# Optimization experiments

Hardware: AMD Instinct MI355X
Metric: run time of the kernel (lower is better)

## Reference

```python
import jax, jax.numpy as jnp
import numpy as np

D = 256      # hidden_dim
NH = 8       # num_heads
DH = D // NH # head_dim = 32
K = 5        # base_kernel -> NA3D kernel (5,5,5), causal on axis 0 (time)
EPS = 1e-6


def _axis_idx(L, k, causal):
    """Per-axis NATTEN neighbor indices [L, k] and validity mask [L, k]."""
    i = jnp.arange(L)
    o = jnp.arange(k)
    if causal:
        idx = i[:, None] - (k - 1) + o[None, :]   # last k positions incl. self
        mask = idx >= 0
        idx = jnp.clip(idx, 0, L - 1)
    else:
        start = jnp.clip(i - k // 2, 0, L - k)     # window shifts at borders
        idx = start[:, None] + o[None, :]
        mask = jnp.ones((L, k), dtype=bool)
    return idx, mask


def _rmsnorm(x, w):
    return x * jax.lax.rsqrt(jnp.mean(x * x, axis=-1, keepdims=True) + EPS) * w


def _na3d(x, wq, bq, wk, bk, wv, bv, wo, bo):
    # x: [B, T, H, W, D]; neighborhood attention, causal in T.
    B, T, H, W, Dm = x.shape
    q = (x @ wq + bq).reshape(B, T, H, W, NH, DH)
    k = (x @ wk + bk).reshape(B, T, H, W, NH, DH)
    v = (x @ wv + bv).reshape(B, T, H, W, NH, DH)

    tidx, tmask = _axis_idx(T, K, True)
    hidx, _ = _axis_idx(H, K, False)
    widx, _ = _axis_idx(W, K, False)

    # Gather neighbor windows: [B, T, H, W, K, K, K, NH, DH]
    ti = tidx[:, None, None, :, None, None]
    hi = hidx[None, :, None, None, :, None]
    wi = widx[None, None, :, None, None, :]
    kn = k[:, ti, hi, wi].reshape(B, T, H, W, K ** 3, NH, DH)
    vn = v[:, ti, hi, wi].reshape(B, T, H, W, K ** 3, NH, DH)

    # Validity mask (only causal time axis masks anything): [T, H, W, K^3]
    mask = jnp.broadcast_to(tmask[:, None, None, :, None, None],
                            (T, H, W, K, K, K)).reshape(T, H, W, K ** 3)

    logits = jnp.einsum('bthwnd,bthwmnd->bthwnm', q, kn) * (DH ** -0.5)
    logits = jnp.where(mask[None, :, :, :, None, :], logits, -jnp.inf)
    attn = jax.nn.softmax(logits, axis=-1)
    out = jnp.einsum('bthwnm,bthwmnd->bthwnd', attn, vn).reshape(B, T, H, W, Dm)
    return out @ wo + bo


def setup_inputs() -> dict:
    key = jax.random.key(0)
    ks = jax.random.split(key, 14)
    w = lambda k_, shape: jax.random.normal(k_, shape, jnp.float32) * 0.02
    return {
        'x': jax.random.normal(ks[0], (1, 8, 16, 16, D), jnp.float32),
        'norm1_w': jnp.ones((D,), jnp.float32),
        'norm2_w': jnp.ones((D,), jnp.float32),
        'wq': w(ks[1], (D, D)), 'bq': jnp.zeros((D,), jnp.float32),
        'wk': w(ks[2], (D, D)), 'bk': jnp.zeros((D,), jnp.float32),
        'wv': w(ks[3], (D, D)), 'bv': jnp.zeros((D,), jnp.float32),
        'wo': w(ks[4], (D, D)), 'bo': jnp.zeros((D,), jnp.float32),
        'w1': w(ks[5], (D, 4 * D)),
        'w2': w(ks[6], (D, 4 * D)),
        'w3': w(ks[7], (4 * D, D)),
    }


def reference(x, norm1_w, norm2_w, wq, bq, wk, bk, wv, bv, wo, bo, w1, w2, w3):
    # residual NA block
    h = x + _na3d(_rmsnorm(x, norm1_w), wq, bq, wk, bk, wv, bv, wo, bo)
    # residual SwiGLU FFN block
    y = _rmsnorm(h, norm2_w)
    h = h + (jax.nn.silu(y @ w1) * (y @ w2)) @ w3
    return h
```

## Files before the change

kernel.cpp:

```cpp
#include <hip/hip_runtime.h>
#include <hip/hip_bf16.h>

typedef __attribute__((ext_vector_type(8))) __bf16 bf16x8;
typedef __attribute__((ext_vector_type(4))) __bf16 bf16x4;
typedef __attribute__((ext_vector_type(4))) short shortx4;
typedef __attribute__((ext_vector_type(4))) float f32x4;

#define D    256
#define FF   1024
#define NTOK 2048

__device__ __forceinline__ float ldf(const void* p, int i, bool isf32){
  return isf32 ? ((const float*)p)[i] : (float)(((const __bf16*)p)[i]);
}

__device__ __forceinline__ f32x4 mfma16x16x16bf16(bf16x4 a, bf16x4 b, f32x4 c){
#if __has_builtin(__builtin_amdgcn_mfma_f32_16x16x16_bf16)
  return __builtin_amdgcn_mfma_f32_16x16x16_bf16(a, b, c, 0, 0, 0);
#elif __has_builtin(__builtin_amdgcn_mfma_f32_16x16x16bf16_1k)
  return __builtin_amdgcn_mfma_f32_16x16x16bf16_1k(__builtin_bit_cast(shortx4, a),
                                                   __builtin_bit_cast(shortx4, b), c, 0, 0, 0);
#else
  asm volatile("v_mfma_f32_16x16x16_bf16 %0, %1, %2, %0" : "+v"(c) : "v"(a), "v"(b));
  return c;
#endif
}

struct MiscArgs { const void* x; const void* vec[6]; };
struct TPArgs { const void* src[7]; };

__global__ __launch_bounds__(256) void prep_kernel(MiscArgs a, TPArgs ta,
                                                   float* __restrict__ X,
                                                   float* __restrict__ VEC,
                                                   __bf16* __restrict__ WT,
                                                   __bf16* __restrict__ XN,
                                                   const unsigned int* __restrict__ tagp){
  __shared__ float tl[32][33];
  __shared__ float red[4];
  bool isf32 = (*tagp == 0x3F800000u);
  int b = blockIdx.x, tid = threadIdx.x;

  if (b < 1024){
    const void* src; int Kd, Nd, dstOff, tk, tn;
    if (b < 256){
      int mat = b >> 6, t = b & 63;
      src = ta.src[mat]; Kd = 256; Nd = 256; dstOff = mat*65536;
      tk = t >> 3; tn = t & 7;
    } else if (b < 768){
      int mat = (b - 256) >> 8, t = (b - 256) & 255;
      src = ta.src[4 + mat]; Kd = 256; Nd = 1024; dstOff = 262144 + mat*262144;
      tk = t >> 5; tn = t & 31;
    } else {
      int t = b - 768;
      src = ta.src[6]; Kd = 1024; Nd = 256; dstOff = 786432;
      tk = t >> 3; tn = t & 7;
    }
    int tx = tid & 31, ty = tid >> 5;
    int k0 = tk*32, n0 = tn*32;
    #pragma unroll
    for (int i = 0; i < 4; i++){
      int kk = ty + i*8;
      tl[kk][tx] = ldf(src, (k0 + kk)*Nd + n0 + tx, isf32);
    }
    __syncthreads();
    #pragma unroll
    for (int i = 0; i < 4; i++){
      int nn = ty + i*8;
      WT[dstOff + (n0 + nn)*Kd + k0 + tx] = (__bf16)tl[tx][nn];
    }
  } else if (b < 3072){
    int tok = b - 1024;
    int idx = tok*D + tid;
    float xv = ldf(a.x, idx, isf32);
    X[idx] = xv;
    float s = xv*xv;
    #pragma unroll
    for (int d = 32; d > 0; d >>= 1) s += __shfl_xor(s, d, 64);
    if ((tid & 63) == 0) red[tid >> 6] = s;
    __syncthreads();
    float tot = red[0]+red[1]+red[2]+red[3];
    float w = ldf(a.vec[0], tid, isf32);
    XN[idx] = (__bf16)(xv * rsqrtf(tot*(1.0f/D) + 1e-6f) * w);
  } else {
    for (int i = tid; i < 1536; i += 256)
      VEC[i] = ldf(a.vec[i >> 8], i & 255, isf32);
  }
}

__global__ __launch_bounds__(256) void rmsnorm_kernel(const float* __restrict__ x,
                                                      const float* __restrict__ w,
                                                      __bf16* __restrict__ out){
  int tok = blockIdx.x, tid = threadIdx.x;
  int idx = tok*D + tid;
  float xv = x[idx];
  float s = xv*xv;
  #pragma unroll
  for (int d = 32; d > 0; d >>= 1) s += __shfl_xor(s, d, 64);
  __shared__ float red[4];
  if ((tid & 63) == 0) red[tid >> 6] = s;
  __syncthreads();
  float tot = red[0]+red[1]+red[2]+red[3];
  out[idx] = (__bf16)(xv * rsqrtf(tot*(1.0f/D) + 1e-6f) * w[tid]);
}


__device__ __forceinline__ void stage256(const __bf16* __restrict__ src, int strideElems,
                                         __bf16* __restrict__ lds){
  int tid = threadIdx.x;
  #pragma unroll
  for (int c = 0; c < 8; c++){
    int s = (c*256 + tid) << 4;
    int row = s >> 9, col = s & 511;
    *(float4*)((char*)lds + row*512 + (col ^ ((row & 7) << 4))) =
      *(const float4*)((const char*)src + row*strideElems*2 + col);
  }
}
__device__ __forceinline__ bf16x8 lrd256(const __bf16* __restrict__ lds, int row, int cb){
  return *(const bf16x8*)((const char*)lds + row*512 + (cb ^ ((row & 7) << 4)));
}

__device__ __forceinline__ void stage128(const __bf16* __restrict__ src, int strideElems,
                                         __bf16* __restrict__ lds){
  int tid = threadIdx.x;
  #pragma unroll
  for (int c = 0; c < 4; c++){
    int s = (c*256 + tid) << 4;
    int row = s >> 8, col = s & 255;
    *(float4*)((char*)lds + row*256 + (col ^ ((row & 7) << 4))) =
      *(const float4*)((const char*)src + row*strideElems*2 + col);
  }
}
__device__ __forceinline__ bf16x8 lrd128(const __bf16* __restrict__ lds, int row, int cb){
  return *(const bf16x8*)((const char*)lds + row*256 + (cb ^ ((row & 7) << 4)));
}

__device__ __forceinline__ void mfma256(const __bf16* __restrict__ As, const __bf16* __restrict__ Bs,
                                        f32x4 acc[2][2], int wrow, int wcol, int q, int ln){
  #pragma unroll
  for (int ks = 0; ks < 8; ks++){
    int cb = ks*64 + q*16;
    bf16x8 a0 = lrd256(As, wrow*32      + ln, cb);
    bf16x8 a1 = lrd256(As, wrow*32 + 16 + ln, cb);
    bf16x8 b0 = lrd256(Bs, wcol*32      + ln, cb);
    bf16x8 b1 = lrd256(Bs, wcol*32 + 16 + ln, cb);
    acc[0][0] = __builtin_amdgcn_mfma_f32_16x16x32_bf16(a0, b0, acc[0][0], 0, 0, 0);
    acc[0][1] = __builtin_amdgcn_mfma_f32_16x16x32_bf16(a0, b1, acc[0][1], 0, 0, 0);
    acc[1][0] = __builtin_amdgcn_mfma_f32_16x16x32_bf16(a1, b0, acc[1][0], 0, 0, 0);
    acc[1][1] = __builtin_amdgcn_mfma_f32_16x16x32_bf16(a1, b1, acc[1][1], 0, 0, 0);
  }
}

#define GEMM_PROLOGUE \
  int tid = threadIdx.x; \
  int wave = tid >> 6, lane = tid & 63; \
  int wrow = wave & 1, wcol = wave >> 1; \
  int q = lane >> 4, ln = lane & 15; \
  (void)tid; \
  f32x4 acc[2][2]; \
  acc[0][0] = (f32x4){0,0,0,0}; acc[0][1] = (f32x4){0,0,0,0}; \
  acc[1][0] = (f32x4){0,0,0,0}; acc[1][1] = (f32x4){0,0,0,0};

__global__ __launch_bounds__(256) void qkv_kernel(const __bf16* __restrict__ xn,
                                                  const __bf16* __restrict__ WT,
                                                  const float* __restrict__ VEC,
                                                  __bf16* __restrict__ Qb,
                                                  __bf16* __restrict__ Kb,
                                                  __bf16* __restrict__ VTb){
  __shared__ __align__(16) __bf16 As[64][256];
  __shared__ __align__(16) __bf16 Bs[64][256];
  int m0 = blockIdx.x*64;
  int sel = blockIdx.y >> 2, n0 = (blockIdx.y & 3)*64;
  const __bf16* B = WT + sel*65536;
  const float* bias = VEC + 512 + sel*256;
  GEMM_PROLOGUE
  stage256(xn + m0*D, D, &As[0][0]);
  stage256(B  + n0*D, D, &Bs[0][0]);
  __syncthreads();
  mfma256(&As[0][0], &Bs[0][0], acc, wrow, wcol, q, ln);
  if (sel < 2){
    __bf16* O = (sel == 0) ? Qb : Kb;
    #pragma unroll
    for (int c = 0; c < 2; c++){
      int col = n0 + wcol*32 + c*16 + ln;
      float bv = bias[col];
      #pragma unroll
      for (int r = 0; r < 2; r++){
        #pragma unroll
        for (int i = 0; i < 4; i++){
          int m = m0 + wrow*32 + r*16 + q*4 + i;
          O[m*D + col] = (__bf16)(acc[r][c][i] + bv);
        }
      }
    }
  } else {
    #pragma unroll
    for (int c = 0; c < 2; c++){
      int col = n0 + wcol*32 + c*16 + ln;
      float bv = bias[col];
      #pragma unroll
      for (int r = 0; r < 2; r++){
        int mb = m0 + wrow*32 + r*16 + q*4;
        bf16x4 pk;
        #pragma unroll
        for (int i = 0; i < 4; i++) pk[i] = (__bf16)(acc[r][c][i] + bv);
        *(bf16x4*)&VTb[col*NTOK + mb] = pk;
      }
    }
  }
}

__global__ __launch_bounds__(256) void attn_kernel(const __bf16* __restrict__ Qb,
                                                   const __bf16* __restrict__ Kb,
                                                   const __bf16* __restrict__ VT,
                                                   __bf16* __restrict__ attn){
  int row = blockIdx.x;
  int tq = row >> 4, hq = row & 15;
  int g  = (blockIdx.y << 2) + (threadIdx.x >> 6);
  int lane = threadIdx.x & 63;
  int ln = lane & 15, qt = lane >> 4;

  int qbase = (tq << 8) + (hq << 4);
  int h0 = min(max(hq - 2, 0), 11);
  int tlo = max(tq - 4, 0);

  bf16x8 qf = *(const bf16x8*)&Qb[(qbase + ln)*D + g*32 + qt*8];

  int wstart = min(max(ln - 2, 0), 11);
  float msk[4];
  #pragma unroll
  for (int r = 0; r < 4; r++){
    int wk = qt*4 + r;
    msk[r] = (wk >= wstart && wk <= wstart + 4) ? 0.0f : -INFINITY;
  }

  const float sc = 0.17677669529663687f;
  float m_run = -INFINITY, l_run = 0.0f;
  f32x4 o0 = (f32x4){0,0,0,0}, o1 = (f32x4){0,0,0,0};
  f32x4 zero = (f32x4){0,0,0,0};

  for (int tp = tlo; tp <= tq; tp++){
    #pragma unroll
    for (int hp = 0; hp < 5; hp++){
      int kb0 = (tp << 8) + ((h0 + hp) << 4);
      bf16x8 kf = *(const bf16x8*)&Kb[(kb0 + ln)*D + g*32 + qt*8];
      f32x4 s = __builtin_amdgcn_mfma_f32_16x16x32_bf16(kf, qf, zero, 0, 0, 0);
      float sv0 = s[0]*sc + msk[0];
      float sv1 = s[1]*sc + msk[1];
      float sv2 = s[2]*sc + msk[2];
      float sv3 = s[3]*sc + msk[3];
      float tm = fmaxf(fmaxf(sv0, sv1), fmaxf(sv2, sv3));
      tm = fmaxf(tm, __shfl_xor(tm, 16, 64));
      tm = fmaxf(tm, __shfl_xor(tm, 32, 64));
      float mnew = fmaxf(m_run, tm);
      float rs = __expf(m_run - mnew);
      float p0 = __expf(sv0 - mnew), p1 = __expf(sv1 - mnew);
      float p2 = __expf(sv2 - mnew), p3 = __expf(sv3 - mnew);
      bf16x4 pa;
      pa[0] = (__bf16)p0; pa[1] = (__bf16)p1; pa[2] = (__bf16)p2; pa[3] = (__bf16)p3;
      l_run = l_run*rs + (float)pa[0] + (float)pa[1] + (float)pa[2] + (float)pa[3];
      #pragma unroll
      for (int i = 0; i < 4; i++){ o0[i] *= rs; o1[i] *= rs; }
      m_run = mnew;
      bf16x4 v0 = *(const bf16x4*)&VT[(g*32      + ln)*NTOK + kb0 + qt*4];
      bf16x4 v1 = *(const bf16x4*)&VT[(g*32 + 16 + ln)*NTOK + kb0 + qt*4];
      o0 = mfma16x16x16bf16(v0, pa, o0);
      o1 = mfma16x16x16bf16(v1, pa, o1);
    }
  }
  l_run += __shfl_xor(l_run, 16, 64);
  l_run += __shfl_xor(l_run, 32, 64);
  float linv = 1.0f / l_run;
  int obase = (qbase + ln)*D + g*32;
  bf16x4 s0, s1;
  #pragma unroll
  for (int r = 0; r < 4; r++){
    s0[r] = (__bf16)(o0[r] * linv);
    s1[r] = (__bf16)(o1[r] * linv);
  }
  *(bf16x4*)&attn[obase      + qt*4] = s0;
  *(bf16x4*)&attn[obase + 16 + qt*4] = s1;
}

__global__ __launch_bounds__(256) void oproj_kernel(const __bf16* __restrict__ A,
                                                    const __bf16* __restrict__ WoT,
                                                    const float* __restrict__ VEC,
                                                    const float* __restrict__ X,
                                                    float* __restrict__ h){
  __shared__ __align__(16) __bf16 As[64][256];
  __shared__ __align__(16) __bf16 Bs[64][256];
  int m0 = blockIdx.x*64, n0 = blockIdx.y*64;
  GEMM_PROLOGUE
  stage256(A   + m0*D, D, &As[0][0]);
  stage256(WoT + n0*D, D, &Bs[0][0]);
  __syncthreads();
  mfma256(&As[0][0], &Bs[0][0], acc, wrow, wcol, q, ln);
  #pragma unroll
  for (int c = 0; c < 2; c++){
    int col = n0 + wcol*32 + c*16 + ln;
    float bv = VEC[1280 + col];
    #pragma unroll
    for (int r = 0; r < 2; r++){
      #pragma unroll
      for (int i = 0; i < 4; i++){
        int m = m0 + wrow*32 + r*16 + q*4 + i;
        int idx = m*D + col;
        h[idx] = acc[r][c][i] + bv + X[idx];
      }
    }
  }
}

__global__ __launch_bounds__(256) void ffn1_kernel(const __bf16* __restrict__ y,
                                                   const __bf16* __restrict__ W1T,
                                                   const __bf16* __restrict__ W2T,
                                                   __bf16* __restrict__ ffh){
  __shared__ __align__(16) __bf16 As [64][128];
  __shared__ __align__(16) __bf16 B1s[64][128];
  __shared__ __align__(16) __bf16 B2s[64][128];
  int m0 = blockIdx.x*64, n0 = blockIdx.y*64;
  int tid = threadIdx.x;
  int wave = tid >> 6, lane = tid & 63;
  int wrow = wave & 1, wcol = wave >> 1;
  int q = lane >> 4, ln = lane & 15;
  f32x4 acc1[2][2], acc2[2][2];
  #pragma unroll
  for (int r = 0; r < 2; r++)
    #pragma unroll
    for (int c = 0; c < 2; c++){ acc1[r][c] = (f32x4){0,0,0,0}; acc2[r][c] = (f32x4){0,0,0,0}; }

  #pragma unroll
  for (int k0 = 0; k0 < D; k0 += 128){
    if (k0) __syncthreads();
    stage128(y   + m0*D + k0, D, &As [0][0]);
    stage128(W1T + n0*D + k0, D, &B1s[0][0]);
    stage128(W2T + n0*D + k0, D, &B2s[0][0]);
    __syncthreads();
    #pragma unroll
    for (int ks = 0; ks < 4; ks++){
      int cb = ks*64 + q*16;
      bf16x8 a0 = lrd128(&As [0][0], wrow*32      + ln, cb);
      bf16x8 a1 = lrd128(&As [0][0], wrow*32 + 16 + ln, cb);
      bf16x8 p0 = lrd128(&B1s[0][0], wcol*32      + ln, cb);
      bf16x8 p1 = lrd128(&B1s[0][0], wcol*32 + 16 + ln, cb);
      bf16x8 u0 = lrd128(&B2s[0][0], wcol*32      + ln, cb);
      bf16x8 u1 = lrd128(&B2s[0][0], wcol*32 + 16 + ln, cb);
      acc1[0][0] = __builtin_amdgcn_mfma_f32_16x16x32_bf16(a0, p0, acc1[0][0], 0,0,0);
      acc1[0][1] = __builtin_amdgcn_mfma_f32_16x16x32_bf16(a0, p1, acc1[0][1], 0,0,0);
      acc1[1][0] = __builtin_amdgcn_mfma_f32_16x16x32_bf16(a1, p0, acc1[1][0], 0,0,0);
      acc1[1][1] = __builtin_amdgcn_mfma_f32_16x16x32_bf16(a1, p1, acc1[1][1], 0,0,0);
      acc2[0][0] = __builtin_amdgcn_mfma_f32_16x16x32_bf16(a0, u0, acc2[0][0], 0,0,0);
      acc2[0][1] = __builtin_amdgcn_mfma_f32_16x16x32_bf16(a0, u1, acc2[0][1], 0,0,0);
      acc2[1][0] = __builtin_amdgcn_mfma_f32_16x16x32_bf16(a1, u0, acc2[1][0], 0,0,0);
      acc2[1][1] = __builtin_amdgcn_mfma_f32_16x16x32_bf16(a1, u1, acc2[1][1], 0,0,0);
    }
  }
  #pragma unroll
  for (int c = 0; c < 2; c++){
    int col = n0 + wcol*32 + c*16 + ln;
    #pragma unroll
    for (int r = 0; r < 2; r++){
      #pragma unroll
      for (int i = 0; i < 4; i++){
        int m = m0 + wrow*32 + r*16 + q*4 + i;
        float gv = acc1[r][c][i], u = acc2[r][c][i];
        float sig = 1.0f / (1.0f + __expf(-gv));
        ffh[m*FF + col] = (__bf16)(gv * sig * u);
      }
    }
  }
}

__global__ __launch_bounds__(256) void ffn2_kernel(const __bf16* __restrict__ ffh,
                                                   const __bf16* __restrict__ W3T,
                                                   const float* __restrict__ h,
                                                   const unsigned int* __restrict__ tagp,
                                                   void* __restrict__ outp){
  __shared__ __align__(16) __bf16 As[64][256];
  __shared__ __align__(16) __bf16 Bs[64][256];
  int m0 = blockIdx.x*64, n0 = blockIdx.y*64;
  GEMM_PROLOGUE
  #pragma unroll
  for (int k0 = 0; k0 < FF; k0 += 256){
    if (k0) __syncthreads();
    stage256(ffh + m0*FF + k0, FF, &As[0][0]);
    stage256(W3T + n0*FF + k0, FF, &Bs[0][0]);
    __syncthreads();
    mfma256(&As[0][0], &Bs[0][0], acc, wrow, wcol, q, ln);
  }
  bool isf32 = (*tagp == 0x3F800000u);
  #pragma unroll
  for (int c = 0; c < 2; c++){
    int col = n0 + wcol*32 + c*16 + ln;
    #pragma unroll
    for (int r = 0; r < 2; r++){
      #pragma unroll
      for (int i = 0; i < 4; i++){
        int m = m0 + wrow*32 + r*16 + q*4 + i;
        int idx = m*D + col;
        float val = acc[r][c][i] + h[idx];
        if (isf32) ((float*)outp)[idx] = val;
        else       ((__bf16*)outp)[idx] = (__bf16)val;
      }
    }
  }
}

extern "C" void kernel_launch(void* const* d_in, const int* in_sizes, int n_in,
                              void* d_out, int out_size, void* d_ws, size_t ws_size,
                              hipStream_t stream){
  char* ws = (char*)d_ws;
  float*  X    = (float*)(ws);
  float*  VEC  = (float*)(ws + 2097152);
  __bf16* WT   = (__bf16*)(ws + 2097152 + 8192);
  __bf16* XN   = (__bf16*)(ws + 4202496);
  __bf16* Qb   = (__bf16*)(ws + 5251072);
  __bf16* Kb   = Qb + NTOK*D;
  __bf16* VTb  = Kb + NTOK*D;
  __bf16* ATT  = (__bf16*)(ws + 11542528);
  float*  Hb   = (float*)(ws + 12591104);
  __bf16* Yb   = (__bf16*)(ws + 14688256);
  __bf16* FFH  = (__bf16*)Qb;

  const unsigned int* tagp = (const unsigned int*)d_in[1];

  MiscArgs ma;
  ma.x = d_in[0];
  ma.vec[0] = d_in[1]; ma.vec[1] = d_in[2]; ma.vec[2] = d_in[4];
  ma.vec[3] = d_in[6]; ma.vec[4] = d_in[8]; ma.vec[5] = d_in[10];

  TPArgs ta;
  ta.src[0] = d_in[3];  ta.src[1] = d_in[5];  ta.src[2] = d_in[7];
  ta.src[3] = d_in[9];  ta.src[4] = d_in[11]; ta.src[5] = d_in[12];
  ta.src[6] = d_in[13];

  prep_kernel<<<3073, 256, 0, stream>>>(ma, ta, X, VEC, WT, XN, tagp);
  qkv_kernel<<<dim3(NTOK/64, 12), 256, 0, stream>>>(XN, WT, VEC, Qb, Kb, VTb);
  attn_kernel<<<dim3(128, 2), 256, 0, stream>>>(Qb, Kb, VTb, ATT);
  oproj_kernel<<<dim3(NTOK/64, 4), 256, 0, stream>>>(ATT, WT + 196608, VEC, X, Hb);
  rmsnorm_kernel<<<NTOK, 256, 0, stream>>>(Hb, VEC + 256, Yb);
  ffn1_kernel<<<dim3(NTOK/64, 16), 256, 0, stream>>>(Yb, WT + 262144, WT + 524288, FFH);
  ffn2_kernel<<<dim3(NTOK/64, 4), 256, 0, stream>>>(FFH, WT + 786432, Hb, tagp, d_out);
}
```

Measured before the change: 135.1 us.

## Fuse all stages into a cooperative persistent megakernel with grid syncs

Replaces the seven separate kernel launches with one cooperative kernel of 512 blocks that runs each stage in turn and separates them with grid-wide barriers. The goal is to remove per-launch overhead and the gaps between launches. In exchange every stage now runs under a fixed grid with 64KB of shared memory per block and launch bounds of 2 blocks per CU, so occupancy may drop. Grid syncs also cost time, and they can leave many blocks idle in stages with fewer tiles. If the cooperative launch fails, it falls back to the separate launches.

Measured after the change: 499.9 us. 270% more time.

```diff
diff --git a/kernel.cpp b/kernel.cpp
--- a/kernel.cpp
+++ b/kernel.cpp
@@ -1,5 +1,8 @@
 #include <hip/hip_runtime.h>
+#include <hip/hip_cooperative_groups.h>
 #include <hip/hip_bf16.h>
+
+namespace cg = cooperative_groups;
 
 typedef __attribute__((ext_vector_type(8))) __bf16 bf16x8;
 typedef __attribute__((ext_vector_type(4))) __bf16 bf16x4;
@@ -29,30 +32,32 @@
 struct MiscArgs { const void* x; const void* vec[6]; };
 struct TPArgs { const void* src[7]; };
 
-__global__ __launch_bounds__(256) void prep_kernel(MiscArgs a, TPArgs ta,
-                                                   float* __restrict__ X,
-                                                   float* __restrict__ VEC,
-                                                   __bf16* __restrict__ WT,
-                                                   __bf16* __restrict__ XN,
-                                                   const unsigned int* __restrict__ tagp){
-  __shared__ float tl[32][33];
-  __shared__ float red[4];
-  bool isf32 = (*tagp == 0x3F800000u);
-  int b = blockIdx.x, tid = threadIdx.x;
-
+struct MegaArgs {
+  MiscArgs ma; TPArgs ta;
+  float* X; float* VEC; __bf16* WT; __bf16* XN;
+  __bf16* Qb; __bf16* Kb; __bf16* VTb; __bf16* ATT;
+  float* Hb; __bf16* Yb; __bf16* FFH;
+  const unsigned int* tagp; void* out;
+};
+
+
+__device__ __forceinline__ void prep_body(const MegaArgs& A, int b, bool isf32, char* smem){
+  float (*tl)[33] = (float(*)[33])smem;
+  float* red = (float*)(smem + 4224);
+  int tid = threadIdx.x;
   if (b < 1024){
     const void* src; int Kd, Nd, dstOff, tk, tn;
     if (b < 256){
       int mat = b >> 6, t = b & 63;
-      src = ta.src[mat]; Kd = 256; Nd = 256; dstOff = mat*65536;
+      src = A.ta.src[mat]; Kd = 256; Nd = 256; dstOff = mat*65536;
       tk = t >> 3; tn = t & 7;
     } else if (b < 768){
       int mat = (b - 256) >> 8, t = (b - 256) & 255;
-      src = ta.src[4 + mat]; Kd = 256; Nd = 1024; dstOff = 262144 + mat*262144;
+      src = A.ta.src[4 + mat]; Kd = 256; Nd = 1024; dstOff = 262144 + mat*262144;
       tk = t >> 5; tn = t & 31;
     } else {
       int t = b - 768;
-      src = ta.src[6]; Kd = 1024; Nd = 256; dstOff = 786432;
+      src = A.ta.src[6]; Kd = 1024; Nd = 256; dstOff = 786432;
       tk = t >> 3; tn = t & 7;
     }
     int tx = tid & 31, ty = tid >> 5;
@@ -66,43 +71,40 @@
     #pragma unroll
     for (int i = 0; i < 4; i++){
       int nn = ty + i*8;
-      WT[dstOff + (n0 + nn)*Kd + k0 + tx] = (__bf16)tl[tx][nn];
+      A.WT[dstOff + (n0 + nn)*Kd + k0 + tx] = (__bf16)tl[tx][nn];
     }
   } else if (b < 3072){
     int tok = b - 1024;
     int idx = tok*D + tid;
-    float xv = ldf(a.x, idx, isf32);
-    X[idx] = xv;
+    float xv = ldf(A.ma.x, idx, isf32);
+    A.X[idx] = xv;
     float s = xv*xv;
     #pragma unroll
     for (int d = 32; d > 0; d >>= 1) s += __shfl_xor(s, d, 64);
     if ((tid & 63) == 0) red[tid >> 6] = s;
     __syncthreads();
     float tot = red[0]+red[1]+red[2]+red[3];
-    float w = ldf(a.vec[0], tid, isf32);
-    XN[idx] = (__bf16)(xv * rsqrtf(tot*(1.0f/D) + 1e-6f) * w);
+    float w = ldf(A.ma.vec[0], tid, isf32);
+    A.XN[idx] = (__bf16)(xv * rsqrtf(tot*(1.0f/D) + 1e-6f) * w);
   } else {
     for (int i = tid; i < 1536; i += 256)
-      VEC[i] = ldf(a.vec[i >> 8], i & 255, isf32);
-  }
-}
-
-__global__ __launch_bounds__(256) void rmsnorm_kernel(const float* __restrict__ x,
-                                                      const float* __restrict__ w,
-                                                      __bf16* __restrict__ out){
-  int tok = blockIdx.x, tid = threadIdx.x;
+      A.VEC[i] = ldf(A.ma.vec[i >> 8], i & 255, isf32);
+  }
+}
+
+__device__ __forceinline__ void rms2_body(const MegaArgs& A, int tok, char* smem){
+  float* red = (float*)smem;
+  int tid = threadIdx.x;
   int idx = tok*D + tid;
-  float xv = x[idx];
+  float xv = A.Hb[idx];
   float s = xv*xv;
   #pragma unroll
   for (int d = 32; d > 0; d >>= 1) s += __shfl_xor(s, d, 64);
-  __shared__ float red[4];
   if ((tid & 63) == 0) red[tid >> 6] = s;
   __syncthreads();
   float tot = red[0]+red[1]+red[2]+red[3];
-  out[idx] = (__bf16)(xv * rsqrtf(tot*(1.0f/D) + 1e-6f) * w[tid]);
-}
-
+  A.Yb[idx] = (__bf16)(xv * rsqrtf(tot*(1.0f/D) + 1e-6f) * A.VEC[256 + tid]);
+}
 
 __device__ __forceinline__ void stage256(const __bf16* __restrict__ src, int strideElems,
                                          __bf16* __restrict__ lds){
@@ -118,7 +120,6 @@
 __device__ __forceinline__ bf16x8 lrd256(const __bf16* __restrict__ lds, int row, int cb){
   return *(const bf16x8*)((const char*)lds + row*512 + (cb ^ ((row & 7) << 4)));
 }
-
 __device__ __forceinline__ void stage128(const __bf16* __restrict__ src, int strideElems,
                                          __bf16* __restrict__ lds){
   int tid = threadIdx.x;
@@ -133,7 +134,6 @@
 __device__ __forceinline__ bf16x8 lrd128(const __bf16* __restrict__ lds, int row, int cb){
   return *(const bf16x8*)((const char*)lds + row*256 + (cb ^ ((row & 7) << 4)));
 }
-
 __device__ __forceinline__ void mfma256(const __bf16* __restrict__ As, const __bf16* __restrict__ Bs,
                                         f32x4 acc[2][2], int wrow, int wcol, int q, int ln){
   #pragma unroll
@@ -160,25 +160,20 @@
   acc[0][0] = (f32x4){0,0,0,0}; acc[0][1] = (f32x4){0,0,0,0}; \
   acc[1][0] = (f32x4){0,0,0,0}; acc[1][1] = (f32x4){0,0,0,0};
 
-__global__ __launch_bounds__(256) void qkv_kernel(const __bf16* __restrict__ xn,
-                                                  const __bf16* __restrict__ WT,
-                                                  const float* __restrict__ VEC,
-                                                  __bf16* __restrict__ Qb,
-                                                  __bf16* __restrict__ Kb,
-                                                  __bf16* __restrict__ VTb){
-  __shared__ __align__(16) __bf16 As[64][256];
-  __shared__ __align__(16) __bf16 Bs[64][256];
-  int m0 = blockIdx.x*64;
-  int sel = blockIdx.y >> 2, n0 = (blockIdx.y & 3)*64;
-  const __bf16* B = WT + sel*65536;
-  const float* bias = VEC + 512 + sel*256;
+__device__ __forceinline__ void qkv_body(const MegaArgs& A, int bx, int by, char* smem){
+  __bf16* As = (__bf16*)smem;
+  __bf16* Bs = (__bf16*)(smem + 32768);
+  int m0 = bx*64;
+  int sel = by >> 2, n0 = (by & 3)*64;
+  const __bf16* B = A.WT + sel*65536;
+  const float* bias = A.VEC + 512 + sel*256;
   GEMM_PROLOGUE
-  stage256(xn + m0*D, D, &As[0][0]);
-  stage256(B  + n0*D, D, &Bs[0][0]);
+  stage256(A.XN + m0*D, D, As);
+  stage256(B    + n0*D, D, Bs);
   __syncthreads();
-  mfma256(&As[0][0], &Bs[0][0], acc, wrow, wcol, q, ln);
+  mfma256(As, Bs, acc, wrow, wcol, q, ln);
   if (sel < 2){
-    __bf16* O = (sel == 0) ? Qb : Kb;
+    __bf16* O = (sel == 0) ? A.Qb : A.Kb;
     #pragma unroll
     for (int c = 0; c < 2; c++){
       int col = n0 + wcol*32 + c*16 + ln;
@@ -203,19 +198,16 @@
         bf16x4 pk;
         #pragma unroll
         for (int i = 0; i < 4; i++) pk[i] = (__bf16)(acc[r][c][i] + bv);
-        *(bf16x4*)&VTb[col*NTOK + mb] = pk;
+        *(bf16x4*)&A.VTb[col*NTOK + mb] = pk;
       }
     }
   }
 }
 
-__global__ __launch_bounds__(256) void attn_kernel(const __bf16* __restrict__ Qb,
-                                                   const __bf16* __restrict__ Kb,
-                                                   const __bf16* __restrict__ VT,
-                                                   __bf16* __restrict__ attn){
-  int row = blockIdx.x;
+__device__ __forceinline__ void attn_body(const MegaArgs& A, int bx, int by){
+  int row = bx;
   int tq = row >> 4, hq = row & 15;
-  int g  = (blockIdx.y << 2) + (threadIdx.x >> 6);
+  int g  = (by << 2) + (threadIdx.x >> 6);
   int lane = threadIdx.x & 63;
   int ln = lane & 15, qt = lane >> 4;
 
@@ -223,7 +215,7 @@
   int h0 = min(max(hq - 2, 0), 11);
   int tlo = max(tq - 4, 0);
 
-  bf16x8 qf = *(const bf16x8*)&Qb[(qbase + ln)*D + g*32 + qt*8];
+  bf16x8 qf = *(const bf16x8*)&A.Qb[(qbase + ln)*D + g*32 + qt*8];
 
   int wstart = min(max(ln - 2, 0), 11);
   float msk[4];
@@ -242,7 +234,7 @@
     #pragma unroll
     for (int hp = 0; hp < 5; hp++){
       int kb0 = (tp << 8) + ((h0 + hp) << 4);
-      bf16x8 kf = *(const bf16x8*)&Kb[(kb0 + ln)*D + g*32 + qt*8];
+      bf16x8 kf = *(const bf16x8*)&A.Kb[(kb0 + ln)*D + g*32 + qt*8];
       f32x4 s = __builtin_amdgcn_mfma_f32_16x16x32_bf16(kf, qf, zero, 0, 0, 0);
       float sv0 = s[0]*sc + msk[0];
       float sv1 = s[1]*sc + msk[1];
@@ -261,8 +253,8 @@
       #pragma unroll
       for (int i = 0; i < 4; i++){ o0[i] *= rs; o1[i] *= rs; }
       m_run = mnew;
-      bf16x4 v0 = *(const bf16x4*)&VT[(g*32      + ln)*NTOK + kb0 + qt*4];
-      bf16x4 v1 = *(const bf16x4*)&VT[(g*32 + 16 + ln)*NTOK + kb0 + qt*4];
+      bf16x4 v0 = *(const bf16x4*)&A.VTb[(g*32      + ln)*NTOK + kb0 + qt*4];
+      bf16x4 v1 = *(const bf16x4*)&A.VTb[(g*32 + 16 + ln)*NTOK + kb0 + qt*4];
       o0 = mfma16x16x16bf16(v0, pa, o0);
       o1 = mfma16x16x16bf16(v1, pa, o1);
     }
@@ -277,47 +269,42 @@
     s0[r] = (__bf16)(o0[r] * linv);
     s1[r] = (__bf16)(o1[r] * linv);
   }
-  *(bf16x4*)&attn[obase      + qt*4] = s0;
-  *(bf16x4*)&attn[obase + 16 + qt*4] = s1;
-}
-
-__global__ __launch_bounds__(256) void oproj_kernel(const __bf16* __restrict__ A,
-                                                    const __bf16* __restrict__ WoT,
-                                                    const float* __restrict__ VEC,
-                                                    const float* __restrict__ X,
-                                                    float* __restrict__ h){
-  __shared__ __align__(16) __bf16 As[64][256];
-  __shared__ __align__(16) __bf16 Bs[64][256];
-  int m0 = blockIdx.x*64, n0 = blockIdx.y*64;
+  *(bf16x4*)&A.ATT[obase      + qt*4] = s0;
+  *(bf16x4*)&A.ATT[obase + 16 + qt*4] = s1;
+}
+
+__device__ __forceinline__ void oproj_body(const MegaArgs& A, int bx, int by, char* smem){
+  __bf16* As = (__bf16*)smem;
+  __bf16* Bs = (__bf16*)(smem + 32768);
+  int m0 = bx*64, n0 = by*64;
   GEMM_PROLOGUE
-  stage256(A   + m0*D, D, &As[0][0]);
-  stage256(WoT + n0*D, D, &Bs[0][0]);
+  stage256(A.ATT + m0*D, D, As);
+  stage256(A.WT + 196608 + n0*D, D, Bs);
   __syncthreads();
-  mfma256(&As[0][0], &Bs[0][0], acc, wrow, wcol, q, ln);
+  mfma256(As, Bs, acc, wrow, wcol, q, ln);
   #pragma unroll
   for (int c = 0; c < 2; c++){
     int col = n0 + wcol*32 + c*16 + ln;
-    float bv = VEC[1280 + col];
+    float bv = A.VEC[1280 + col];
     #pragma unroll
     for (int r = 0; r < 2; r++){
       #pragma unroll
       for (int i = 0; i < 4; i++){
         int m = m0 + wrow*32 + r*16 + q*4 + i;
         int idx = m*D + col;
-        h[idx] = acc[r][c][i] + bv + X[idx];
+        A.Hb[idx] = acc[r][c][i] + bv + A.X[idx];
       }
     }
   }
 }
 
-__global__ __launch_bounds__(256) void ffn1_kernel(const __bf16* __restrict__ y,
-                                                   const __bf16* __restrict__ W1T,
-                                                   const __bf16* __restrict__ W2T,
-                                                   __bf16* __restrict__ ffh){
-  __shared__ __align__(16) __bf16 As [64][128];
-  __shared__ __align__(16) __bf16 B1s[64][128];
-  __shared__ __align__(16) __bf16 B2s[64][128];
-  int m0 = blockIdx.x*64, n0 = blockIdx.y*64;
+__device__ __forceinline__ void ffn1_body(const MegaArgs& A, int bx, int by, char* smem){
+  __bf16* As  = (__bf16*)smem;
+  __bf16* B1s = (__bf16*)(smem + 16384);
+  __bf16* B2s = (__bf16*)(smem + 32768);
+  const __bf16* W1T = A.WT + 262144;
+  const __bf16* W2T = A.WT + 524288;
+  int m0 = bx*64, n0 = by*64;
   int tid = threadIdx.x;
   int wave = tid >> 6, lane = tid & 63;
   int wrow = wave & 1, wcol = wave >> 1;
@@ -331,19 +318,19 @@
   #pragma unroll
   for (int k0 = 0; k0 < D; k0 += 128){
     if (k0) __syncthreads();
-    stage128(y   + m0*D + k0, D, &As [0][0]);
-    stage128(W1T + n0*D + k0, D, &B1s[0][0]);
-    stage128(W2T + n0*D + k0, D, &B2s[0][0]);
+    stage128(A.Yb + m0*D + k0, D, As);
+    stage128(W1T  + n0*D + k0, D, B1s);
+    stage128(W2T  + n0*D + k0, D, B2s);
     __syncthreads();
     #pragma unroll
     for (int ks = 0; ks < 4; ks++){
       int cb = ks*64 + q*16;
-      bf16x8 a0 = lrd128(&As [0][0], wrow*32      + ln, cb);
-      bf16x8 a1 = lrd128(&As [0][0], wrow*32 + 16 + ln, cb);
-      bf16x8 p0 = lrd128(&B1s[0][0], wcol*32      + ln, cb);
-      bf16x8 p1 = lrd128(&B1s[0][0], wcol*32 + 16 + ln, cb);
-      bf16x8 u0 = lrd128(&B2s[0][0], wcol*32      + ln, cb);
-      bf16x8 u1 = lrd128(&B2s[0][0], wcol*32 + 16 + ln, cb);
+      bf16x8 a0 = lrd128(As,  wrow*32      + ln, cb);
+      bf16x8 a1 = lrd128(As,  wrow*32 + 16 + ln, cb);
+      bf16x8 p0 = lrd128(B1s, wcol*32      + ln, cb);
+      bf16x8 p1 = lrd128(B1s, wcol*32 + 16 + ln, cb);
+      bf16x8 u0 = lrd128(B2s, wcol*32      + ln, cb);
+      bf16x8 u1 = lrd128(B2s, wcol*32 + 16 + ln, cb);
       acc1[0][0] = __builtin_amdgcn_mfma_f32_16x16x32_bf16(a0, p0, acc1[0][0], 0,0,0);
       acc1[0][1] = __builtin_amdgcn_mfma_f32_16x16x32_bf16(a0, p1, acc1[0][1], 0,0,0);
       acc1[1][0] = __builtin_amdgcn_mfma_f32_16x16x32_bf16(a1, p0, acc1[1][0], 0,0,0);
@@ -364,30 +351,26 @@
         int m = m0 + wrow*32 + r*16 + q*4 + i;
         float gv = acc1[r][c][i], u = acc2[r][c][i];
         float sig = 1.0f / (1.0f + __expf(-gv));
-        ffh[m*FF + col] = (__bf16)(gv * sig * u);
+        A.FFH[m*FF + col] = (__bf16)(gv * sig * u);
       }
     }
   }
 }
 
-__global__ __launch_bounds__(256) void ffn2_kernel(const __bf16* __restrict__ ffh,
-                                                   const __bf16* __restrict__ W3T,
-                                                   const float* __restrict__ h,
-                                                   const unsigned int* __restrict__ tagp,
-                                                   void* __restrict__ outp){
-  __shared__ __align__(16) __bf16 As[64][256];
-  __shared__ __align__(16) __bf16 Bs[64][256];
-  int m0 = blockIdx.x*64, n0 = blockIdx.y*64;
+__device__ __forceinline__ void ffn2_body(const MegaArgs& A, int bx, int by, char* smem, bool isf32){
+  __bf16* As = (__bf16*)smem;
+  __bf16* Bs = (__bf16*)(smem + 32768);
+  const __bf16* W3T = A.WT + 786432;
+  int m0 = bx*64, n0 = by*64;
   GEMM_PROLOGUE
   #pragma unroll
   for (int k0 = 0; k0 < FF; k0 += 256){
     if (k0) __syncthreads();
-    stage256(ffh + m0*FF + k0, FF, &As[0][0]);
-    stage256(W3T + n0*FF + k0, FF, &Bs[0][0]);
-    __syncthreads();
-    mfma256(&As[0][0], &Bs[0][0], acc, wrow, wcol, q, ln);
-  }
-  bool isf32 = (*tagp == 0x3F800000u);
+    stage256(A.FFH + m0*FF + k0, FF, As);
+    stage256(W3T   + n0*FF + k0, FF, Bs);
+    __syncthreads();
+    mfma256(As, Bs, acc, wrow, wcol, q, ln);
+  }
   #pragma unroll
   for (int c = 0; c < 2; c++){
     int col = n0 + wcol*32 + c*16 + ln;
@@ -397,47 +380,107 @@
       for (int i = 0; i < 4; i++){
         int m = m0 + wrow*32 + r*16 + q*4 + i;
         int idx = m*D + col;
-        float val = acc[r][c][i] + h[idx];
-        if (isf32) ((float*)outp)[idx] = val;
-        else       ((__bf16*)outp)[idx] = (__bf16)val;
+        float val = acc[r][c][i] + A.Hb[idx];
+        if (isf32) ((float*)A.out)[idx] = val;
+        else       ((__bf16*)A.out)[idx] = (__bf16)val;
       }
     }
   }
+}
+
+__global__ __launch_bounds__(256, 2) void mega_kernel(MegaArgs A){
+  cg::grid_group grid = cg::this_grid();
+  __shared__ __align__(16) char smem[65536];
+  bool isf32 = (*A.tagp == 0x3F800000u);
+  int nb = gridDim.x;
+  for (int b = blockIdx.x; b < 3073; b += nb){
+    prep_body(A, b, isf32, smem);
+    __syncthreads();
+  }
+  grid.sync();
+  if (blockIdx.x < 384) qkv_body(A, blockIdx.x & 31, blockIdx.x >> 5, smem);
+  grid.sync();
+  if (blockIdx.x < 256) attn_body(A, blockIdx.x & 127, blockIdx.x >> 7);
+  grid.sync();
+  if (blockIdx.x < 128) oproj_body(A, blockIdx.x & 31, blockIdx.x >> 5, smem);
+  grid.sync();
+  for (int b = blockIdx.x; b < 2048; b += nb){
+    rms2_body(A, b, smem);
+    __syncthreads();
+  }
+  grid.sync();
+  if (blockIdx.x < 512) ffn1_body(A, blockIdx.x & 31, blockIdx.x >> 5, smem);
+  grid.sync();
+  if (blockIdx.x < 128) ffn2_body(A, blockIdx.x & 31, blockIdx.x >> 5, smem, isf32);
+}
+
+__global__ __launch_bounds__(256) void prep_kernel(MegaArgs A){
+  __shared__ __align__(16) char smem[4608];
+  bool isf32 = (*A.tagp == 0x3F800000u);
+  prep_body(A, blockIdx.x, isf32, smem);
+}
+__global__ __launch_bounds__(256) void qkv_kernel(MegaArgs A){
+  __shared__ __align__(16) char smem[65536];
+  qkv_body(A, blockIdx.x, blockIdx.y, smem);
+}
+__global__ __launch_bounds__(256) void attn_kernel(MegaArgs A){
+  attn_body(A, blockIdx.x, blockIdx.y);
+}
+__global__ __launch_bounds__(256) void oproj_kernel(MegaArgs A){
+  __shared__ __align__(16) char smem[65536];
+  oproj_body(A, blockIdx.x, blockIdx.y, smem);
+}
+__global__ __launch_bounds__(256) void rms2_kernel(MegaArgs A){
+  __shared__ __align__(16) char smem[16];
+  rms2_body(A, blockIdx.x, smem);
+}
+__global__ __launch_bounds__(256) void ffn1_kernel(MegaArgs A){
+  __shared__ __align__(16) char smem[49152];
+  ffn1_body(A, blockIdx.x, blockIdx.y, smem);
+}
+__global__ __launch_bounds__(256) void ffn2_kernel(MegaArgs A){
+  __shared__ __align__(16) char smem[65536];
+  bool isf32 = (*A.tagp == 0x3F800000u);
+  ffn2_body(A, blockIdx.x, blockIdx.y, smem, isf32);
 }
 
 extern "C" void kernel_launch(void* const* d_in, const int* in_sizes, int n_in,
                               void* d_out, int out_size, void* d_ws, size_t ws_size,
                               hipStream_t stream){
   char* ws = (char*)d_ws;
-  float*  X    = (float*)(ws);
-  float*  VEC  = (float*)(ws + 2097152);
-  __bf16* WT   = (__bf16*)(ws + 2097152 + 8192);
-  __bf16* XN   = (__bf16*)(ws + 4202496);
-  __bf16* Qb   = (__bf16*)(ws + 5251072);
-  __bf16* Kb   = Qb + NTOK*D;
-  __bf16* VTb  = Kb + NTOK*D;
-  __bf16* ATT  = (__bf16*)(ws + 11542528);
-  float*  Hb   = (float*)(ws + 12591104);
-  __bf16* Yb   = (__bf16*)(ws + 14688256);
-  __bf16* FFH  = (__bf16*)Qb;
-
-  const unsigned int* tagp = (const unsigned int*)d_in[1];
-
-  MiscArgs ma;
-  ma.x = d_in[0];
-  ma.vec[0] = d_in[1]; ma.vec[1] = d_in[2]; ma.vec[2] = d_in[4];
-  ma.vec[3] = d_in[6]; ma.vec[4] = d_in[8]; ma.vec[5] = d_in[10];
-
-  TPArgs ta;
-  ta.src[0] = d_in[3];  ta.src[1] = d_in[5];  ta.src[2] = d_in[7];
-  ta.src[3] = d_in[9];  ta.src[4] = d_in[11]; ta.src[5] = d_in[12];
-  ta.src[6] = d_in[13];
-
-  prep_kernel<<<3073, 256, 0, stream>>>(ma, ta, X, VEC, WT, XN, tagp);
-  qkv_kernel<<<dim3(NTOK/64, 12), 256, 0, stream>>>(XN, WT, VEC, Qb, Kb, VTb);
-  attn_kernel<<<dim3(128, 2), 256, 0, stream>>>(Qb, Kb, VTb, ATT);
-  oproj_kernel<<<dim3(NTOK/64, 4), 256, 0, stream>>>(ATT, WT + 196608, VEC, X, Hb);
-  rmsnorm_kernel<<<NTOK, 256, 0, stream>>>(Hb, VEC + 256, Yb);
-  ffn1_kernel<<<dim3(NTOK/64, 16), 256, 0, stream>>>(Yb, WT + 262144, WT + 524288, FFH);
-  ffn2_kernel<<<dim3(NTOK/64, 4), 256, 0, stream>>>(FFH, WT + 786432, Hb, tagp, d_out);
-}
+  MegaArgs A;
+  A.X    = (float*)(ws);
+  A.VEC  = (float*)(ws + 2097152);
+  A.WT   = (__bf16*)(ws + 2097152 + 8192);
+  A.XN   = (__bf16*)(ws + 4202496);
+  A.Qb   = (__bf16*)(ws + 5251072);
+  A.Kb   = A.Qb + NTOK*D;
+  A.VTb  = A.Kb + NTOK*D;
+  A.ATT  = (__bf16*)(ws + 11542528);
+  A.Hb   = (float*)(ws + 12591104);
+  A.Yb   = (__bf16*)(ws + 14688256);
+  A.FFH  = A.Qb;
+  A.tagp = (const unsigned int*)d_in[1];
+  A.out  = d_out;
+
+  A.ma.x = d_in[0];
+  A.ma.vec[0] = d_in[1]; A.ma.vec[1] = d_in[2]; A.ma.vec[2] = d_in[4];
+  A.ma.vec[3] = d_in[6]; A.ma.vec[4] = d_in[8]; A.ma.vec[5] = d_in[10];
+
+  A.ta.src[0] = d_in[3];  A.ta.src[1] = d_in[5];  A.ta.src[2] = d_in[7];
+  A.ta.src[3] = d_in[9];  A.ta.src[4] = d_in[11]; A.ta.src[5] = d_in[12];
+  A.ta.src[6] = d_in[13];
+
+  void* kargs[] = { (void*)&A };
+  hipError_t err = hipLaunchCooperativeKernel((void*)mega_kernel, dim3(512), dim3(256),
+                                              kargs, 0u, stream);
+  if (err != hipSuccess){
+    prep_kernel<<<3073, 256, 0, stream>>>(A);
+    qkv_kernel<<<dim3(32, 12), 256, 0, stream>>>(A);
+    attn_kernel<<<dim3(128, 2), 256, 0, stream>>>(A);
+    oproj_kernel<<<dim3(32, 4), 256, 0, stream>>>(A);
+    rms2_kernel<<<2048, 256, 0, stream>>>(A);
+    ffn1_kernel<<<dim3(32, 16), 256, 0, stream>>>(A);
+    ffn2_kernel<<<dim3(32, 4), 256, 0, stream>>>(A);
+  }
+}
```
